# Performance work log

Measured on AMD Instinct MI355X. Metric: run time of the kernel, lower is better.

The kernel has to match this reference:

```python
import jax, jax.numpy as jnp
import numpy as np

B, C_IN, C_OUT, H, W = 16, 32, 32, 256, 256
M1, M2 = 32, 32  # kept Fourier modes (kbase // 2**level)


def setup_inputs() -> dict:
    key = jax.random.key(0)
    ks = jax.random.split(key, 7)
    scale = 1.0 / (C_IN * C_OUT)
    return {
        "x": jax.random.normal(ks[0], (B, C_IN, H, W), dtype=jnp.float32),
        "conv_w": jax.random.normal(ks[1], (C_OUT, 3 * C_IN), dtype=jnp.float32) * (1.0 / np.sqrt(3 * C_IN)),
        "conv_b": jax.random.normal(ks[2], (C_OUT,), dtype=jnp.float32) * 0.01,
        "w1r": jax.random.normal(ks[3], (C_IN, C_OUT, M1, M2), dtype=jnp.float32) * scale,
        "w1i": jax.random.normal(ks[4], (C_IN, C_OUT, M1, M2), dtype=jnp.float32) * scale,
        "w2r": jax.random.normal(ks[5], (C_IN, C_OUT, M1, M2), dtype=jnp.float32) * scale,
        "w2i": jax.random.normal(ks[6], (C_IN, C_OUT, M1, M2), dtype=jnp.float32) * scale,
    }


def _combi_forward(x, conv_w, conv_b, w1r, w1i, w2r, w2i):
    # ---- diff branch: EasyDiffs (x, forward-diff along H, forward-diff along W) + 1x1 conv ----
    zrow = jnp.zeros_like(x[:, :, :1, :])
    zcol = jnp.zeros_like(x[:, :, :, :1])
    dh = jnp.concatenate([x[:, :, 1:, :] - x[:, :, :-1, :], zrow], axis=2)  # [B,C,H,W]
    dw = jnp.concatenate([x[:, :, :, 1:] - x[:, :, :, :-1], zcol], axis=3)  # [B,C,H,W]
    feats = jnp.concatenate([x, dh, dw], axis=1)  # [B,3C,H,W]
    diff_out = jnp.einsum("bchw,oc->bohw", feats, conv_w) + conv_b[None, :, None, None]

    # ---- spectral branch: rfft2 -> truncated complex multiply (two corners) -> irfft2 ----
    xf = jnp.fft.rfft2(x, axes=(-2, -1))  # [B,C,H,W//2+1] complex
    w1 = w1r + 1j * w1i
    w2 = w2r + 1j * w2i
    top = jnp.einsum("bixy,ioxy->boxy", xf[:, :, :M1, :M2], w1)
    bot = jnp.einsum("bixy,ioxy->boxy", xf[:, :, -M1:, :M2], w2)
    out_ft = jnp.zeros((B, C_OUT, H, W // 2 + 1), dtype=xf.dtype)
    out_ft = out_ft.at[:, :, :M1, :M2].set(top)
    out_ft = out_ft.at[:, :, -M1:, :M2].set(bot)
    fno_out = jnp.fft.irfft2(out_ft, s=(H, W), axes=(-2, -1))

    return diff_out + fno_out


def reference(x, conv_w, conv_b, w1r, w1i, w2r, w2i):
    return _combi_forward(x, conv_w, conv_b, w1r, w1i, w2r, w2i)
```

## Files before the change

kernel.cpp:

```cpp
#include <hip/hip_runtime.h>


#define PI2_256 0.02454369260617026f

__device__ __forceinline__ unsigned short bf16r(float f) {
    unsigned u = __float_as_uint(f);
    u += 0x7fffu + ((u >> 16) & 1u);
    return (unsigned short)(u >> 16);
}
__device__ __forceinline__ float bf16tof(unsigned short h) {
    return __uint_as_float((unsigned)h << 16);
}
__device__ __forceinline__ unsigned pack2(float a, float b) {
    return (unsigned)bf16r(a) | ((unsigned)bf16r(b) << 16);
}

typedef __attribute__((ext_vector_type(8))) short short8;
typedef __attribute__((ext_vector_type(4))) float float4v;

__global__ __launch_bounds__(256) void k_twiddle(float* __restrict__ ws) {
    unsigned short* E = (unsigned short*)(ws + 8388608);
    int idx0 = blockIdx.x * 256 + threadIdx.x;
    for (int idx = idx0; idx < 4 * 64 * 72; idx += 16 * 256) {
        int c = idx / 4608;
        int rem = idx - c * 4608;
        int col = rem / 72;
        int wp = rem - col * 72;
        unsigned short hi = 0, lo = 0;
        if (wp < 64) {
            int w = c * 64 + wp;
            int ky = col & 31;
            int prod = (ky * w) & 255;
            float s, cc;
            __sincosf(PI2_256 * (float)prod, &s, &cc);
            float val = (col < 32) ? cc : -s;
            hi = bf16r(val);
            lo = bf16r(val - bf16tof(hi));
        }
        E[c * 9216 + col * 72 + wp] = hi;
        E[c * 9216 + 4608 + col * 72 + wp] = lo;
    }
}

__global__ __launch_bounds__(256) void k_dftw(const float* __restrict__ x,
                                              const float* __restrict__ Ews,
                                              float* __restrict__ Ar,
                                              float* __restrict__ Ai) {
    __shared__ __align__(16) unsigned char smem[55296];
    unsigned short* Xhi = (unsigned short*)smem;
    unsigned short* Xlo = (unsigned short*)(smem + 18432);
    unsigned short* Ehi = (unsigned short*)(smem + 36864);
    float* obuf = (float*)smem;

    int t = threadIdx.x;
    int bc = blockIdx.x >> 1;
    int h0 = (blockIdx.x & 1) << 7;
    int lane = t & 63, wid = t >> 6;
    int quad = lane >> 4, col = lane & 15;

    const uint4* Ews4 = (const uint4*)Ews;

    float4v zero = {0.f, 0.f, 0.f, 0.f};
    float4v acc[4][2];
#pragma unroll
    for (int m = 0; m < 4; ++m) {
        acc[m][0] = zero;
        acc[m][1] = zero;
    }

    for (int c = 0; c < 4; ++c) {
        const float* xrow = x + ((size_t)bc * 256 + h0) * 256 + c * 64;
#pragma unroll
        for (int it = 0; it < 8; ++it) {
            int l = it * 256 + t;
            int r = l >> 4, f4 = l & 15;
            float4 v = *(const float4*)(xrow + (size_t)r * 256 + f4 * 4);
            unsigned short hx = bf16r(v.x), hy = bf16r(v.y);
            unsigned short hz = bf16r(v.z), hw = bf16r(v.w);
            unsigned hi0 = (unsigned)hx | ((unsigned)hy << 16);
            unsigned hi1 = (unsigned)hz | ((unsigned)hw << 16);
            unsigned lo0 = (unsigned)bf16r(v.x - bf16tof(hx)) |
                           ((unsigned)bf16r(v.y - bf16tof(hy)) << 16);
            unsigned lo1 = (unsigned)bf16r(v.z - bf16tof(hz)) |
                           ((unsigned)bf16r(v.w - bf16tof(hw)) << 16);
            int o = r * 72 + f4 * 4;
            *(uint2*)&Xhi[o] = make_uint2(hi0, hi1);
            *(uint2*)&Xlo[o] = make_uint2(lo0, lo1);
        }
        for (int g = t; g < 1152; g += 256)
            ((uint4*)(smem + 36864))[g] = Ews4[c * 1152 + g];
        __syncthreads();

#pragma unroll
        for (int ks = 0; ks < 2; ++ks) {
            int ko = quad * 8 + ks * 32;
            short8 ah[4], al[4], bh[2], bl[2];
#pragma unroll
            for (int m = 0; m < 4; ++m) {
                int ro = (m * 16 + col) * 72 + ko;
                ah[m] = *(const short8*)&Ehi[ro];
                al[m] = *(const short8*)&Ehi[4608 + ro];
            }
#pragma unroll
            for (int n = 0; n < 2; ++n) {
                int hr = ((wid * 2 + n) * 16 + col) * 72 + ko;
                bh[n] = *(const short8*)&Xhi[hr];
                bl[n] = *(const short8*)&Xlo[hr];
            }
#pragma unroll
            for (int m = 0; m < 4; ++m) {
#pragma unroll
                for (int n = 0; n < 2; ++n) {
                    acc[m][n] = __builtin_amdgcn_mfma_f32_16x16x32_bf16(ah[m], bh[n], acc[m][n], 0, 0, 0);
                    acc[m][n] = __builtin_amdgcn_mfma_f32_16x16x32_bf16(ah[m], bl[n], acc[m][n], 0, 0, 0);
                    acc[m][n] = __builtin_amdgcn_mfma_f32_16x16x32_bf16(al[m], bh[n], acc[m][n], 0, 0, 0);
                }
            }
        }
        __syncthreads();
    }

#pragma unroll
    for (int m = 0; m < 4; ++m) {
#pragma unroll
        for (int n = 0; n < 2; ++n) {
            int hl = (wid * 2 + n) * 16 + col;
            *(float4v*)&obuf[hl * 68 + m * 16 + quad * 4] = acc[m][n];
        }
    }
    __syncthreads();
#pragma unroll
    for (int it = 0; it < 8; ++it) {
        int l = it * 256 + t;
        int hh = l >> 4, f = l & 15;
        float4 v = *(float4*)&obuf[hh * 68 + f * 4];
        size_t g = (size_t)bc * 8192 + (size_t)(h0 + hh) * 32;
        if (f < 8) *(float4*)(Ar + g + f * 4) = v;
        else       *(float4*)(Ai + g + (f - 8) * 4) = v;
    }
}

__global__ __launch_bounds__(256) void k_dfth(const float* __restrict__ Ar,
                                              const float* __restrict__ Ai,
                                              float* __restrict__ xfr,
                                              float* __restrict__ xfi) {
    __shared__ __align__(16) float asr[256 * 32];
    __shared__ __align__(16) float asi[256 * 32];
    __shared__ __align__(16) float ob[64 * 33];
    int t = threadIdx.x;
    int bc = blockIdx.x;
    const float4* sr = (const float4*)(Ar + (size_t)bc * 8192);
    const float4* si = (const float4*)(Ai + (size_t)bc * 8192);
#pragma unroll
    for (int it = 0; it < 8; ++it) {
        ((float4*)asr)[it * 256 + t] = sr[it * 256 + t];
        ((float4*)asi)[it * 256 + t] = si[it * 256 + t];
    }
    __syncthreads();

    int kxi = t & 63, kg = t >> 6;
    int kx = (kxi < 32) ? kxi : kxi + 192;
    float c1, s1;
    __sincosf(PI2_256 * (float)kx, &s1, &c1);
    float c = 1.f, s = 0.f;
    float xr[8] = {0, 0, 0, 0, 0, 0, 0, 0};
    float xi_[8] = {0, 0, 0, 0, 0, 0, 0, 0};
    for (int h = 0; h < 256; ++h) {
        float4 a0 = *(float4*)&asr[h * 32 + kg * 8];
        float4 a1 = *(float4*)&asr[h * 32 + kg * 8 + 4];
        float4 b0 = *(float4*)&asi[h * 32 + kg * 8];
        float4 b1 = *(float4*)&asi[h * 32 + kg * 8 + 4];
        float arv[8] = {a0.x, a0.y, a0.z, a0.w, a1.x, a1.y, a1.z, a1.w};
        float aiv[8] = {b0.x, b0.y, b0.z, b0.w, b1.x, b1.y, b1.z, b1.w};
#pragma unroll
        for (int j = 0; j < 8; ++j) {
            xr[j] += arv[j] * c + aiv[j] * s;
            xi_[j] += aiv[j] * c - arv[j] * s;
        }
        float nc = c * c1 - s * s1;
        s = s * c1 + c * s1;
        c = nc;
    }
#pragma unroll
    for (int j = 0; j < 8; ++j) ob[kxi * 33 + kg * 8 + j] = xr[j];
    __syncthreads();
#pragma unroll
    for (int it = 0; it < 8; ++it) {
        int l = it * 256 + t;
        xfr[(size_t)bc * 2048 + l] = ob[(l >> 5) * 33 + (l & 31)];
    }
    __syncthreads();
#pragma unroll
    for (int j = 0; j < 8; ++j) ob[kxi * 33 + kg * 8 + j] = xi_[j];
    __syncthreads();
#pragma unroll
    for (int it = 0; it < 8; ++it) {
        int l = it * 256 + t;
        xfi[(size_t)bc * 2048 + l] = ob[(l >> 5) * 33 + (l & 31)];
    }
}

__global__ __launch_bounds__(256) void k_mix(float* __restrict__ xfr,
                                             float* __restrict__ xfi,
                                             const float* __restrict__ w1r,
                                             const float* __restrict__ w1i,
                                             const float* __restrict__ w2r,
                                             const float* __restrict__ w2i) {
    __shared__ float wr[32 * 32 * 8];
    __shared__ float wi[32 * 32 * 8];
    __shared__ float xsr[32 * 8];
    __shared__ float xsi[32 * 8];
    int t = threadIdx.x;
    int kxi = (blockIdx.x >> 2) & 63;
    int ky0 = (blockIdx.x & 3) * 8;
    int b0 = (blockIdx.x >> 8) * 4;
    const float* Wr = (kxi < 32) ? w1r : w2r;
    const float* Wi = (kxi < 32) ? w1i : w2i;
    int m1 = kxi & 31;
#pragma unroll
    for (int it = 0; it < 32; ++it) {
        int l = it * 256 + t;
        int i = l >> 8, o = (l >> 3) & 31, q = l & 7;
        size_t g = (size_t)i * 32768 + (size_t)o * 1024 + m1 * 32 + ky0 + q;
        wr[l] = Wr[g];
        wi[l] = Wi[g];
    }
    __syncthreads();

    int o = t >> 3, q = t & 7;
    for (int b = b0; b < b0 + 4; ++b) {
        __syncthreads();
        {
            int i = t >> 3, qq = t & 7;
            size_t g = ((size_t)(b * 32 + i)) * 2048 + (size_t)kxi * 32 + ky0 + qq;
            xsr[t] = xfr[g];
            xsi[t] = xfi[g];
        }
        __syncthreads();
        float accr = 0.f, acci = 0.f;
#pragma unroll
        for (int i = 0; i < 32; ++i) {
            float xr = xsr[i * 8 + q], xim = xsi[i * 8 + q];
            float wrv = wr[i * 256 + o * 8 + q], wiv = wi[i * 256 + o * 8 + q];
            accr += xr * wrv - xim * wiv;
            acci += xr * wiv + xim * wrv;
        }
        size_t g = ((size_t)(b * 32 + o)) * 2048 + (size_t)kxi * 32 + ky0 + q;
        xfr[g] = accr;
        xfi[g] = acci;
    }
}

__global__ __launch_bounds__(256) void k_idfth(const float* __restrict__ ofr,
                                               const float* __restrict__ ofi,
                                               float* __restrict__ T) {
    __shared__ __align__(16) float osr[64 * 32];
    __shared__ __align__(16) float osi[64 * 32];
    __shared__ __align__(16) float obT[64 * 64];
    int t = threadIdx.x;
    int bo = blockIdx.x;
#pragma unroll
    for (int it = 0; it < 2; ++it) {
        ((float4*)osr)[it * 256 + t] = ((const float4*)(ofr + (size_t)bo * 2048))[it * 256 + t];
        ((float4*)osi)[it * 256 + t] = ((const float4*)(ofi + (size_t)bo * 2048))[it * 256 + t];
    }
    __syncthreads();

    int ky = t & 31, hg = t >> 5;
    float sc = ((ky == 0) ? 1.f : 2.f) * (1.f / 65536.f);
    for (int hc = 0; hc < 4; ++hc) {
        float tr[8] = {0, 0, 0, 0, 0, 0, 0, 0}, ti[8] = {0, 0, 0, 0, 0, 0, 0, 0};
        float cc[8], ss[8], ca[8], sa[8];
#pragma unroll
        for (int j = 0; j < 8; ++j) {
            int h = hc * 64 + hg * 8 + j;
            __sincosf(PI2_256 * (float)h, &sa[j], &ca[j]);
            cc[j] = 1.f;
            ss[j] = 0.f;
        }
        for (int kxi = 0; kxi < 32; ++kxi) {
            float orv = osr[kxi * 32 + ky], oiv = osi[kxi * 32 + ky];
#pragma unroll
            for (int j = 0; j < 8; ++j) {
                tr[j] += orv * cc[j] - oiv * ss[j];
                ti[j] += orv * ss[j] + oiv * cc[j];
                float nc = cc[j] * ca[j] - ss[j] * sa[j];
                ss[j] = ss[j] * ca[j] + cc[j] * sa[j];
                cc[j] = nc;
            }
        }
#pragma unroll
        for (int j = 0; j < 8; ++j) {
            int h = hc * 64 + hg * 8 + j;
            int m = (224 * h) & 255;
            __sincosf(PI2_256 * (float)m, &ss[j], &cc[j]);
        }
        for (int kxi = 32; kxi < 64; ++kxi) {
            float orv = osr[kxi * 32 + ky], oiv = osi[kxi * 32 + ky];
#pragma unroll
            for (int j = 0; j < 8; ++j) {
                tr[j] += orv * cc[j] - oiv * ss[j];
                ti[j] += orv * ss[j] + oiv * cc[j];
                float nc = cc[j] * ca[j] - ss[j] * sa[j];
                ss[j] = ss[j] * ca[j] + cc[j] * sa[j];
                cc[j] = nc;
            }
        }
        __syncthreads();
#pragma unroll
        for (int j = 0; j < 8; ++j) {
            int hl = hg * 8 + j;
            obT[hl * 64 + 2 * ky] = tr[j] * sc;
            obT[hl * 64 + 2 * ky + 1] = ti[j] * sc;
        }
        __syncthreads();
        float* dst = T + (size_t)bo * 16384 + hc * 4096;
#pragma unroll
        for (int it = 0; it < 4; ++it)
            ((float4*)dst)[it * 256 + t] = ((float4*)obT)[it * 256 + t];
    }
}

#define BT_PITCH 164

__global__ __launch_bounds__(256) void k_final(const float* __restrict__ x,
                                               const float* __restrict__ cw,
                                               const float* __restrict__ cb,
                                               const float* __restrict__ T,
                                               float* __restrict__ out) {
    __shared__ unsigned short Bt[128 * BT_PITCH];
    __shared__ __align__(16) unsigned short Afr[5 * 2 * 64 * 8];

    int t = threadIdx.x;
    int b = blockIdx.x >> 9;
    int h = (blockIdx.x >> 1) & 255;
    int w0 = (blockIdx.x & 1) << 7;

    {
        int nn = t & 127, half = t >> 7;
        int w = w0 + nn;
        int hs = (h < 255) ? h + 1 : h;
        int we = (w < 255) ? 1 : 0;
#pragma unroll
        for (int ip = 0; ip < 8; ++ip) {
            int i0 = half * 16 + ip * 2;
            const float* x0 = x + ((size_t)(b * 32 + i0)) * 65536;
            const float* x1 = x0 + 65536;
            float c0 = x0[h * 256 + w];
            float s0 = x0[hs * 256 + w];
            float e0 = x0[h * 256 + w + we];
            float c1 = x1[h * 256 + w];
            float s1 = x1[hs * 256 + w];
            float e1 = x1[h * 256 + w + we];
            *(unsigned*)&Bt[nn * BT_PITCH + i0]      = pack2(c0, c1);
            *(unsigned*)&Bt[nn * BT_PITCH + 32 + i0] = pack2(s0 - c0, s1 - c1);
            *(unsigned*)&Bt[nn * BT_PITCH + 64 + i0] = pack2(e0 - c0, e1 - c1);
        }
    }
    {
        int nn = t & 127, half = t >> 7;
        int w = w0 + nn;
        float c1, s1;
        __sincosf(PI2_256 * (float)w, &s1, &c1);
        int kk0 = half * 16;
        float c, s;
        __sincosf(PI2_256 * (float)((w * kk0) & 255), &s, &c);
#pragma unroll
        for (int kp = 0; kp < 8; ++kp) {
            int kk = kk0 + kp * 2;
            float ca = c, sa = s;
            float nc = c * c1 - s * s1; s = s * c1 + c * s1; c = nc;
            float cbv = c, sbv = s;
            nc = c * c1 - s * s1; s = s * c1 + c * s1; c = nc;
            *(unsigned*)&Bt[nn * BT_PITCH + 96 + kk]  = pack2(ca, cbv);
            *(unsigned*)&Bt[nn * BT_PITCH + 128 + kk] = pack2(-sa, -sbv);
        }
    }
    for (int slot = t; slot < 640; slot += 256) {
        int ks = slot >> 7;
        int mt = (slot >> 6) & 1;
        int lane = slot & 63;
        int m = (lane & 15) + mt * 16;
        int kb = ks * 32 + (lane >> 4) * 8;
        float v[8];
        if (ks < 3) {
#pragma unroll
            for (int j = 0; j < 8; ++j) v[j] = cw[m * 96 + kb + j];
        } else {
            const float* tp = T + ((size_t)(b * 32 + m)) * 16384 + (size_t)h * 64;
            int kkb = kb - (ks == 3 ? 96 : 128);
            int im = (ks == 3) ? 0 : 1;
#pragma unroll
            for (int j = 0; j < 8; ++j) v[j] = tp[2 * (kkb + j) + im];
        }
        uint4 pk;
        pk.x = pack2(v[0], v[1]); pk.y = pack2(v[2], v[3]);
        pk.z = pack2(v[4], v[5]); pk.w = pack2(v[6], v[7]);
        *(uint4*)&Afr[((ks * 2 + mt) * 64 + lane) * 8] = pk;
    }
    __syncthreads();

    int lane = t & 63, wid = t >> 6;
    int quad = lane >> 4, col = lane & 15;
    float4v zero = {0.f, 0.f, 0.f, 0.f};
    float4v acc[2][2];
    acc[0][0] = zero; acc[0][1] = zero; acc[1][0] = zero; acc[1][1] = zero;

#pragma unroll
    for (int ks = 0; ks < 5; ++ks) {
        short8 a0 = *(const short8*)&Afr[((ks * 2 + 0) * 64 + lane) * 8];
        short8 a1 = *(const short8*)&Afr[((ks * 2 + 1) * 64 + lane) * 8];
        int kb = ks * 32 + quad * 8;
        union { unsigned long long q[2]; short8 v; } ub0, ub1;
        const unsigned short* r0 = &Bt[(wid * 32 + col) * BT_PITCH + kb];
        const unsigned short* r1 = &Bt[(wid * 32 + 16 + col) * BT_PITCH + kb];
        ub0.q[0] = *(const unsigned long long*)(r0);
        ub0.q[1] = *(const unsigned long long*)(r0 + 4);
        ub1.q[0] = *(const unsigned long long*)(r1);
        ub1.q[1] = *(const unsigned long long*)(r1 + 4);
        acc[0][0] = __builtin_amdgcn_mfma_f32_16x16x32_bf16(a0, ub0.v, acc[0][0], 0, 0, 0);
        acc[1][0] = __builtin_amdgcn_mfma_f32_16x16x32_bf16(a1, ub0.v, acc[1][0], 0, 0, 0);
        acc[0][1] = __builtin_amdgcn_mfma_f32_16x16x32_bf16(a0, ub1.v, acc[0][1], 0, 0, 0);
        acc[1][1] = __builtin_amdgcn_mfma_f32_16x16x32_bf16(a1, ub1.v, acc[1][1], 0, 0, 0);
    }

#pragma unroll
    for (int mt = 0; mt < 2; ++mt) {
#pragma unroll
        for (int nt = 0; nt < 2; ++nt) {
#pragma unroll
            for (int reg = 0; reg < 4; ++reg) {
                int o = mt * 16 + quad * 4 + reg;
                int w = w0 + wid * 32 + nt * 16 + col;
                out[(((size_t)(b * 32 + o)) * 256 + h) * 256 + w] = acc[mt][nt][reg] + cb[o];
            }
        }
    }
}

extern "C" void kernel_launch(void* const* d_in, const int* in_sizes, int n_in,
                              void* d_out, int out_size, void* d_ws, size_t ws_size,
                              hipStream_t stream) {
    const float* x = (const float*)d_in[0];
    const float* conv_w = (const float*)d_in[1];
    const float* conv_b = (const float*)d_in[2];
    const float* w1r = (const float*)d_in[3];
    const float* w1i = (const float*)d_in[4];
    const float* w2r = (const float*)d_in[5];
    const float* w2i = (const float*)d_in[6];
    float* out = (float*)d_out;

    float* ws = (float*)d_ws;
    float* Ar = ws;
    float* Ai = ws + 4194304;
    float* Tbuf = ws;
    float* xfr = ws + 8388608;
    float* xfi = ws + 9437184;
    const float* Ews = ws + 8388608;

    k_twiddle<<<16, 256, 0, stream>>>(ws);
    k_dftw<<<1024, 256, 0, stream>>>(x, Ews, Ar, Ai);
    k_dfth<<<512, 256, 0, stream>>>(Ar, Ai, xfr, xfi);
    k_mix<<<1024, 256, 0, stream>>>(xfr, xfi, w1r, w1i, w2r, w2i);
    k_idfth<<<512, 256, 0, stream>>>(xfr, xfi, Tbuf);
    k_final<<<8192, 256, 0, stream>>>(x, conv_w, conv_b, Tbuf, out);
}
```

Before: 514.5 us.

## Move H-direction forward and inverse DFTs onto bf16x3 MFMA

```diff
diff --git a/kernel.cpp b/kernel.cpp
--- a/kernel.cpp
+++ b/kernel.cpp
@@ -140,63 +140,112 @@
     }
 }
 
+#define DF_PITCH 72
+
 __global__ __launch_bounds__(256) void k_dfth(const float* __restrict__ Ar,
                                               const float* __restrict__ Ai,
                                               float* __restrict__ xfr,
                                               float* __restrict__ xfi) {
-    __shared__ __align__(16) float asr[256 * 32];
-    __shared__ __align__(16) float asi[256 * 32];
-    __shared__ __align__(16) float ob[64 * 33];
+    __shared__ __align__(16) unsigned short F2h[128 * DF_PITCH];
+    __shared__ __align__(16) unsigned short F2l[128 * DF_PITCH];
+    __shared__ __align__(16) unsigned short B2h[32 * DF_PITCH];
+    __shared__ __align__(16) unsigned short B2l[32 * DF_PITCH];
+
     int t = threadIdx.x;
     int bc = blockIdx.x;
-    const float4* sr = (const float4*)(Ar + (size_t)bc * 8192);
-    const float4* si = (const float4*)(Ai + (size_t)bc * 8192);
-#pragma unroll
-    for (int it = 0; it < 8; ++it) {
-        ((float4*)asr)[it * 256 + t] = sr[it * 256 + t];
-        ((float4*)asi)[it * 256 + t] = si[it * 256 + t];
-    }
-    __syncthreads();
-
-    int kxi = t & 63, kg = t >> 6;
+    int lane = t & 63, wid = t >> 6;
+    int quad = lane >> 4, col = lane & 15;
+
+    int m = t & 127;
+    int kxi = m >> 1;
     int kx = (kxi < 32) ? kxi : kxi + 192;
+    int neg = m & 1;
+    int khalf = t >> 7;
     float c1, s1;
     __sincosf(PI2_256 * (float)kx, &s1, &c1);
-    float c = 1.f, s = 0.f;
-    float xr[8] = {0, 0, 0, 0, 0, 0, 0, 0};
-    float xi_[8] = {0, 0, 0, 0, 0, 0, 0, 0};
-    for (int h = 0; h < 256; ++h) {
-        float4 a0 = *(float4*)&asr[h * 32 + kg * 8];
-        float4 a1 = *(float4*)&asr[h * 32 + kg * 8 + 4];
-        float4 b0 = *(float4*)&asi[h * 32 + kg * 8];
-        float4 b1 = *(float4*)&asi[h * 32 + kg * 8 + 4];
-        float arv[8] = {a0.x, a0.y, a0.z, a0.w, a1.x, a1.y, a1.z, a1.w};
-        float aiv[8] = {b0.x, b0.y, b0.z, b0.w, b1.x, b1.y, b1.z, b1.w};
-#pragma unroll
-        for (int j = 0; j < 8; ++j) {
-            xr[j] += arv[j] * c + aiv[j] * s;
-            xi_[j] += aiv[j] * c - arv[j] * s;
-        }
-        float nc = c * c1 - s * s1;
-        s = s * c1 + c * s1;
-        c = nc;
-    }
-#pragma unroll
-    for (int j = 0; j < 8; ++j) ob[kxi * 33 + kg * 8 + j] = xr[j];
-    __syncthreads();
-#pragma unroll
-    for (int it = 0; it < 8; ++it) {
-        int l = it * 256 + t;
-        xfr[(size_t)bc * 2048 + l] = ob[(l >> 5) * 33 + (l & 31)];
-    }
-    __syncthreads();
-#pragma unroll
-    for (int j = 0; j < 8; ++j) ob[kxi * 33 + kg * 8 + j] = xi_[j];
-    __syncthreads();
-#pragma unroll
-    for (int it = 0; it < 8; ++it) {
-        int l = it * 256 + t;
-        xfi[(size_t)bc * 2048 + l] = ob[(l >> 5) * 33 + (l & 31)];
+
+    float4v zero = {0.f, 0.f, 0.f, 0.f};
+    float4v acc[2][2];
+    acc[0][0] = zero; acc[0][1] = zero; acc[1][0] = zero; acc[1][1] = zero;
+
+    for (int hc = 0; hc < 8; ++hc) {
+        {
+            int h0 = hc * 32 + khalf * 16;
+            float c, s;
+            __sincosf(PI2_256 * (float)((kx * h0) & 255), &s, &c);
+#pragma unroll
+            for (int j = 0; j < 16; ++j) {
+                int kk = 2 * (khalf * 16 + j);
+                float ch = bf16tof(bf16r(c)), sh = bf16tof(bf16r(s));
+                float cl = c - ch, sl = s - sh;
+                unsigned hiw, low;
+                if (neg == 0) { hiw = pack2(c, s);  low = pack2(cl, sl); }
+                else          { hiw = pack2(-s, c); low = pack2(-sl, cl); }
+                *(unsigned*)&F2h[m * DF_PITCH + kk] = hiw;
+                *(unsigned*)&F2l[m * DF_PITCH + kk] = low;
+                float nc = c * c1 - s * s1;
+                s = s * c1 + c * s1;
+                c = nc;
+            }
+        }
+        {
+            int hl = t >> 3;
+            int ky0 = (t & 7) * 4;
+            const float* pr = Ar + (size_t)bc * 8192 + (size_t)(hc * 32 + hl) * 32 + ky0;
+            const float* pi = Ai + (size_t)bc * 8192 + (size_t)(hc * 32 + hl) * 32 + ky0;
+            float4 vr = *(const float4*)pr;
+            float4 vi = *(const float4*)pi;
+            float fr[4] = {vr.x, vr.y, vr.z, vr.w};
+            float fi[4] = {vi.x, vi.y, vi.z, vi.w};
+#pragma unroll
+            for (int q = 0; q < 4; ++q) {
+                float ar = fr[q], ai = fi[q];
+                float arh = bf16tof(bf16r(ar)), aih = bf16tof(bf16r(ai));
+                *(unsigned*)&B2h[(ky0 + q) * DF_PITCH + 2 * hl] = pack2(ar, ai);
+                *(unsigned*)&B2l[(ky0 + q) * DF_PITCH + 2 * hl] = pack2(ar - arh, ai - aih);
+            }
+        }
+        __syncthreads();
+#pragma unroll
+        for (int ks = 0; ks < 2; ++ks) {
+            int ko = ks * 32 + quad * 8;
+            short8 ah[2], al[2], bh[2], bl[2];
+#pragma unroll
+            for (int mi = 0; mi < 2; ++mi) {
+                int ro = ((wid * 2 + mi) * 16 + col) * DF_PITCH + ko;
+                ah[mi] = *(const short8*)&F2h[ro];
+                al[mi] = *(const short8*)&F2l[ro];
+            }
+#pragma unroll
+            for (int ni = 0; ni < 2; ++ni) {
+                int ro = (ni * 16 + col) * DF_PITCH + ko;
+                bh[ni] = *(const short8*)&B2h[ro];
+                bl[ni] = *(const short8*)&B2l[ro];
+            }
+#pragma unroll
+            for (int mi = 0; mi < 2; ++mi) {
+#pragma unroll
+                for (int ni = 0; ni < 2; ++ni) {
+                    acc[mi][ni] = __builtin_amdgcn_mfma_f32_16x16x32_bf16(ah[mi], bh[ni], acc[mi][ni], 0, 0, 0);
+                    acc[mi][ni] = __builtin_amdgcn_mfma_f32_16x16x32_bf16(ah[mi], bl[ni], acc[mi][ni], 0, 0, 0);
+                    acc[mi][ni] = __builtin_amdgcn_mfma_f32_16x16x32_bf16(al[mi], bh[ni], acc[mi][ni], 0, 0, 0);
+                }
+            }
+        }
+        __syncthreads();
+    }
+#pragma unroll
+    for (int mi = 0; mi < 2; ++mi) {
+#pragma unroll
+        for (int ni = 0; ni < 2; ++ni) {
+#pragma unroll
+            for (int reg = 0; reg < 4; ++reg) {
+                int mm = (wid * 2 + mi) * 16 + quad * 4 + reg;
+                size_t g = (size_t)bc * 2048 + (size_t)(mm >> 1) * 32 + ni * 16 + col;
+                if (mm & 1) xfi[g] = acc[mi][ni][reg];
+                else        xfr[g] = acc[mi][ni][reg];
+            }
+        }
     }
 }
 
@@ -251,73 +300,96 @@
     }
 }
 
+#define IF_PITCH 136
+
 __global__ __launch_bounds__(256) void k_idfth(const float* __restrict__ ofr,
                                                const float* __restrict__ ofi,
                                                float* __restrict__ T) {
-    __shared__ __align__(16) float osr[64 * 32];
-    __shared__ __align__(16) float osi[64 * 32];
-    __shared__ __align__(16) float obT[64 * 64];
+    __shared__ __align__(16) unsigned short Fh[64 * IF_PITCH];
+    __shared__ __align__(16) unsigned short Fl[64 * IF_PITCH];
+    __shared__ __align__(16) unsigned short Gh[64 * IF_PITCH];
+    __shared__ __align__(16) unsigned short Gl[64 * IF_PITCH];
+
     int t = threadIdx.x;
     int bo = blockIdx.x;
-#pragma unroll
-    for (int it = 0; it < 2; ++it) {
-        ((float4*)osr)[it * 256 + t] = ((const float4*)(ofr + (size_t)bo * 2048))[it * 256 + t];
-        ((float4*)osi)[it * 256 + t] = ((const float4*)(ofi + (size_t)bo * 2048))[it * 256 + t];
-    }
-    __syncthreads();
-
-    int ky = t & 31, hg = t >> 5;
-    float sc = ((ky == 0) ? 1.f : 2.f) * (1.f / 65536.f);
+    int lane = t & 63, wid = t >> 6;
+    int quad = lane >> 4, col = lane & 15;
+
+    {
+        int kxi = t >> 2;
+        int ky0 = (t & 3) * 8;
+        const float* pr = ofr + (size_t)bo * 2048 + (size_t)kxi * 32 + ky0;
+        const float* pi = ofi + (size_t)bo * 2048 + (size_t)kxi * 32 + ky0;
+        float4 r0 = *(const float4*)pr, r1 = *(const float4*)(pr + 4);
+        float4 i0 = *(const float4*)pi, i1 = *(const float4*)(pi + 4);
+        float fr[8] = {r0.x, r0.y, r0.z, r0.w, r1.x, r1.y, r1.z, r1.w};
+        float fi[8] = {i0.x, i0.y, i0.z, i0.w, i1.x, i1.y, i1.z, i1.w};
+#pragma unroll
+        for (int q = 0; q < 8; ++q) {
+            int ky = ky0 + q;
+            float sc = ((ky == 0) ? 1.f : 2.f) * (1.f / 65536.f);
+            float vr = fr[q] * sc, vi = fi[q] * sc;
+            float vrh = bf16tof(bf16r(vr)), vih = bf16tof(bf16r(vi));
+            float vrl = vr - vrh, vil = vi - vih;
+            *(unsigned*)&Gh[(2 * ky) * IF_PITCH + 2 * kxi]     = pack2(vr, -vi);
+            *(unsigned*)&Gh[(2 * ky + 1) * IF_PITCH + 2 * kxi] = pack2(vi, vr);
+            *(unsigned*)&Gl[(2 * ky) * IF_PITCH + 2 * kxi]     = pack2(vrl, -vil);
+            *(unsigned*)&Gl[(2 * ky + 1) * IF_PITCH + 2 * kxi] = pack2(vil, vrl);
+        }
+    }
+
+    int hl_ = t & 63;
+    int g = t >> 6;
+    int kxi0 = g * 16;
+    int kx0 = (g < 2) ? kxi0 : kxi0 + 192;
+
     for (int hc = 0; hc < 4; ++hc) {
-        float tr[8] = {0, 0, 0, 0, 0, 0, 0, 0}, ti[8] = {0, 0, 0, 0, 0, 0, 0, 0};
-        float cc[8], ss[8], ca[8], sa[8];
-#pragma unroll
-        for (int j = 0; j < 8; ++j) {
-            int h = hc * 64 + hg * 8 + j;
-            __sincosf(PI2_256 * (float)h, &sa[j], &ca[j]);
-            cc[j] = 1.f;
-            ss[j] = 0.f;
-        }
-        for (int kxi = 0; kxi < 32; ++kxi) {
-            float orv = osr[kxi * 32 + ky], oiv = osi[kxi * 32 + ky];
-#pragma unroll
-            for (int j = 0; j < 8; ++j) {
-                tr[j] += orv * cc[j] - oiv * ss[j];
-                ti[j] += orv * ss[j] + oiv * cc[j];
-                float nc = cc[j] * ca[j] - ss[j] * sa[j];
-                ss[j] = ss[j] * ca[j] + cc[j] * sa[j];
-                cc[j] = nc;
-            }
-        }
-#pragma unroll
-        for (int j = 0; j < 8; ++j) {
-            int h = hc * 64 + hg * 8 + j;
-            int m = (224 * h) & 255;
-            __sincosf(PI2_256 * (float)m, &ss[j], &cc[j]);
-        }
-        for (int kxi = 32; kxi < 64; ++kxi) {
-            float orv = osr[kxi * 32 + ky], oiv = osi[kxi * 32 + ky];
-#pragma unroll
-            for (int j = 0; j < 8; ++j) {
-                tr[j] += orv * cc[j] - oiv * ss[j];
-                ti[j] += orv * ss[j] + oiv * cc[j];
-                float nc = cc[j] * ca[j] - ss[j] * sa[j];
-                ss[j] = ss[j] * ca[j] + cc[j] * sa[j];
-                cc[j] = nc;
-            }
-        }
-        __syncthreads();
-#pragma unroll
-        for (int j = 0; j < 8; ++j) {
-            int hl = hg * 8 + j;
-            obT[hl * 64 + 2 * ky] = tr[j] * sc;
-            obT[hl * 64 + 2 * ky + 1] = ti[j] * sc;
-        }
-        __syncthreads();
-        float* dst = T + (size_t)bo * 16384 + hc * 4096;
-#pragma unroll
-        for (int it = 0; it < 4; ++it)
-            ((float4*)dst)[it * 256 + t] = ((float4*)obT)[it * 256 + t];
+        int h = hc * 64 + hl_;
+        {
+            float c1, s1;
+            __sincosf(PI2_256 * (float)h, &s1, &c1);
+            float c, s;
+            __sincosf(PI2_256 * (float)((kx0 * h) & 255), &s, &c);
+#pragma unroll
+            for (int j = 0; j < 16; ++j) {
+                int kk = 2 * (kxi0 + j);
+                float ch = bf16tof(bf16r(c)), sh = bf16tof(bf16r(s));
+                *(unsigned*)&Fh[hl_ * IF_PITCH + kk] = pack2(c, s);
+                *(unsigned*)&Fl[hl_ * IF_PITCH + kk] = pack2(c - ch, s - sh);
+                float nc = c * c1 - s * s1;
+                s = s * c1 + c * s1;
+                c = nc;
+            }
+        }
+        __syncthreads();
+        float4v zero = {0.f, 0.f, 0.f, 0.f};
+        float4v acc[4];
+        acc[0] = zero; acc[1] = zero; acc[2] = zero; acc[3] = zero;
+#pragma unroll
+        for (int ks = 0; ks < 4; ++ks) {
+            int ko = ks * 32 + quad * 8;
+            short8 bh = *(const short8*)&Gh[(wid * 16 + col) * IF_PITCH + ko];
+            short8 bl = *(const short8*)&Gl[(wid * 16 + col) * IF_PITCH + ko];
+#pragma unroll
+            for (int mt = 0; mt < 4; ++mt) {
+                int ro = (mt * 16 + col) * IF_PITCH + ko;
+                short8 ah = *(const short8*)&Fh[ro];
+                short8 al = *(const short8*)&Fl[ro];
+                acc[mt] = __builtin_amdgcn_mfma_f32_16x16x32_bf16(ah, bh, acc[mt], 0, 0, 0);
+                acc[mt] = __builtin_amdgcn_mfma_f32_16x16x32_bf16(ah, bl, acc[mt], 0, 0, 0);
+                acc[mt] = __builtin_amdgcn_mfma_f32_16x16x32_bf16(al, bh, acc[mt], 0, 0, 0);
+            }
+        }
+        float* dst = T + (size_t)bo * 16384 + (size_t)hc * 4096;
+#pragma unroll
+        for (int mt = 0; mt < 4; ++mt) {
+#pragma unroll
+            for (int reg = 0; reg < 4; ++reg) {
+                int hh = mt * 16 + quad * 4 + reg;
+                dst[hh * 64 + wid * 16 + col] = acc[mt][reg];
+            }
+        }
+        __syncthreads();
     }
 }
 
```

Result: faster. 431.8 us (-16.1%).
